# Kernel tuning notes

Hardware: AMD Instinct MI355X
Metric: run time of the kernel (lower is better)

Reference implementation:

```python
import jax, jax.numpy as jnp
import numpy as np
import math

N_HEADS = 16

def _layernorm(x, g, b):
    m = x.mean(-1, keepdims=True)
    v = ((x - m) ** 2).mean(-1, keepdims=True)
    return (x - m) * jax.lax.rsqrt(v + 1e-5) * g + b

def _project(x):
    # Poincare ball (c=1) projection: clip last-dim norm to 1 - eps
    max_norm = 1.0 - 1e-5
    n = jnp.linalg.norm(x, axis=-1, keepdims=True)
    return jnp.where(n > max_norm, x * (max_norm / jnp.maximum(n, 1e-12)), x)


def setup_inputs() -> dict:
    key = jax.random.key(0)
    ks = jax.random.split(key, 8)
    B, L, D = 2, 2048, 1024
    w = lambda k, s: jax.random.normal(k, s, jnp.float32) * 0.02
    return dict(
        x=jax.random.normal(ks[0], (B, L, D), jnp.float32),
        wq=w(ks[1], (D, D)), bq=jnp.zeros((D,), jnp.float32),
        wk=w(ks[2], (D, D)), bk=jnp.zeros((D,), jnp.float32),
        wv=w(ks[3], (D, D)), bv=jnp.zeros((D,), jnp.float32),
        wo=w(ks[4], (D, D)), bo=jnp.zeros((D,), jnp.float32),
        g1=jnp.ones((D,), jnp.float32), b1=jnp.zeros((D,), jnp.float32),
        g2=jnp.ones((D,), jnp.float32), b2=jnp.zeros((D,), jnp.float32),
        w1=w(ks[5], (4 * D, D)), bf1=jnp.zeros((4 * D,), jnp.float32),
        w2=w(ks[6], (D, 4 * D)), bf2=jnp.zeros((D,), jnp.float32),
    )


def reference(x, wq, bq, wk, bk, wv, bv, wo, bo, g1, b1, g2, b2, w1, bf1, w2, bf2):
    B, L, D = x.shape
    H = N_HEADS
    hd = D // H
    temp = math.sqrt(hd)

    xn = _layernorm(x, g1, b1)

    def heads(w, b):
        y = xn @ w.T + b                       # [B, L, D]
        return y.reshape(B, L, H, hd).transpose(0, 2, 1, 3)  # [B, H, L, hd]

    q = _project(heads(wq, bq))
    k = _project(heads(wk, bk))
    v = heads(wv, bv)

    # -||q - k||^2 / temp, via ||q||^2 + ||k||^2 - 2 q.k (same math as the
    # explicit broadcast-diff in the torch code, expressed as a GEMM)
    q2 = (q ** 2).sum(-1)[..., :, None]        # [B, H, L, 1]
    k2 = (k ** 2).sum(-1)[..., None, :]        # [B, H, 1, L]
    qk = jnp.einsum('bhld,bhmd->bhlm', q, k)   # [B, H, L, L]
    scores = -(q2 + k2 - 2.0 * qk) / temp
    attn = jax.nn.softmax(scores, axis=-1)     # dropout = identity (eval mode)

    out = jnp.einsum('bhlm,bhmd->bhld', attn, v)
    out = out.transpose(0, 2, 1, 3).reshape(B, L, D) @ wo.T + bo

    x = _project(x + out)
    xn2 = _layernorm(x, g2, b2)
    h = jax.nn.gelu(xn2 @ w1.T + bf1, approximate=False)  # torch nn.GELU = erf
    x = _project(x + (h @ w2.T + bf2))
    return x
```

## Files before the change

### kernel.cpp

```cpp
#include <hip/hip_runtime.h>
#include <math.h>

#define SEQ_L 2048
#define DM    1024
#define NH    16
#define HD    64
#define BL    4096
#define DFF   4096
#define QKV_S 3072

typedef __attribute__((ext_vector_type(8))) short short8;
typedef __attribute__((ext_vector_type(4))) short s16x4;
typedef __attribute__((ext_vector_type(4))) float f32x4;

__device__ __forceinline__ short f2bf(float x) {
    unsigned u = __float_as_uint(x);
    u += 0x7fff + ((u >> 16) & 1);
    return (short)(u >> 16);
}
__device__ __forceinline__ float bf2f(short s) {
    return __uint_as_float(((unsigned)(unsigned short)s) << 16);
}

__device__ __forceinline__ float gelu_fast(float x) {
    const float xa = fabsf(x);
    const float z = xa * 0.70710678118654752440f;
    const float t = __builtin_amdgcn_rcpf(fmaf(0.3275911f, z, 1.f));
    float P = fmaf(t, 1.061405429f, -1.453152027f);
    P = fmaf(t, P, 1.421413741f);
    P = fmaf(t, P, -0.284496736f);
    P = fmaf(t, P, 0.254829592f);
    P *= t;
    const float e = __expf(-z * z);
    const float erfp = fmaf(-P, e, 1.f);
    return 0.5f * fmaf(xa, erfp, x);
}

__device__ __forceinline__ float block_sum(float v, float* red, int tid) {
#pragma unroll
    for (int m = 32; m; m >>= 1) v += __shfl_xor(v, m);
    if ((tid & 63) == 0) red[tid >> 6] = v;
    __syncthreads();
    v = red[0] + red[1] + red[2] + red[3];
    __syncthreads();
    return v;
}

__global__ __launch_bounds__(256) void cvt6_kernel(
    const float* __restrict__ wq, const float* __restrict__ wk,
    const float* __restrict__ wv, const float* __restrict__ wo,
    const float* __restrict__ w1, const float* __restrict__ w2,
    short* __restrict__ dst) {
    const size_t i = (size_t)blockIdx.x * 256 + threadIdx.x;
    const float* src;
    size_t off;
    if (i < 1048576) {
        const int seg = (int)(i >> 18);
        off = i & 262143;
        src = seg == 0 ? wq : seg == 1 ? wk : seg == 2 ? wv : wo;
    } else if (i < 2097152) { src = w1; off = i - 1048576; }
    else                    { src = w2; off = i - 2097152; }
    const float4 v = ((const float4*)src)[off];
    const s16x4 o = {f2bf(v.x), f2bf(v.y), f2bf(v.z), f2bf(v.w)};
    ((s16x4*)dst)[i] = o;
}

__global__ __launch_bounds__(256) void ln_bf16_kernel(const float* __restrict__ x,
                                                      const float* __restrict__ g,
                                                      const float* __restrict__ b,
                                                      short* __restrict__ out) {
    const int row = blockIdx.x;
    const int tid = threadIdx.x;
    __shared__ float red[4];
    const float4 xv = *(const float4*)(x + (size_t)row * DM + tid * 4);
    float s = xv.x + xv.y + xv.z + xv.w;
    s = block_sum(s, red, tid);
    const float mean = s * (1.f / (float)DM);
    float dx0 = xv.x - mean, dx1 = xv.y - mean, dx2 = xv.z - mean, dx3 = xv.w - mean;
    float ss = dx0 * dx0 + dx1 * dx1 + dx2 * dx2 + dx3 * dx3;
    ss = block_sum(ss, red, tid);
    const float rs = 1.f / sqrtf(ss * (1.f / (float)DM) + 1e-5f);
    const float4 gv = *(const float4*)(g + tid * 4);
    const float4 bv = *(const float4*)(b + tid * 4);
    const s16x4 ob = {f2bf(dx0 * rs * gv.x + bv.x), f2bf(dx1 * rs * gv.y + bv.y),
                      f2bf(dx2 * rs * gv.z + bv.z), f2bf(dx3 * rs * gv.w + bv.w)};
    *(s16x4*)(out + (size_t)row * DM + tid * 4) = ob;
}

__global__ __launch_bounds__(256) void resproj3_kernel(const float* __restrict__ a,
                                                       const float* __restrict__ c0,
                                                       const float* __restrict__ c1,
                                                       float* __restrict__ out) {
    const int row = blockIdx.x;
    const int tid = threadIdx.x;
    __shared__ float red[4];
    const float4 av = *(const float4*)(a + (size_t)row * DM + tid * 4);
    const float4 c0v = *(const float4*)(c0 + (size_t)row * DM + tid * 4);
    const float4 c1v = *(const float4*)(c1 + (size_t)row * DM + tid * 4);
    float4 sv;
    sv.x = av.x + c0v.x + c1v.x;
    sv.y = av.y + c0v.y + c1v.y;
    sv.z = av.z + c0v.z + c1v.z;
    sv.w = av.w + c0v.w + c1v.w;
    float ss = sv.x * sv.x + sv.y * sv.y + sv.z * sv.z + sv.w * sv.w;
    ss = block_sum(ss, red, tid);
    const float n = sqrtf(ss);
    const float mx = 1.f - 1e-5f;
    const float scale = (n > mx) ? (mx / fmaxf(n, 1e-12f)) : 1.f;
    sv.x *= scale; sv.y *= scale; sv.z *= scale; sv.w *= scale;
    *(float4*)(out + (size_t)row * DM + tid * 4) = sv;
}

__global__ __launch_bounds__(256) void qk_prep(const short* __restrict__ qkvB,
                                               short* __restrict__ Qb,
                                               short* __restrict__ Kb,
                                               float* __restrict__ k2) {
    const int tid = threadIdx.x, lane = tid & 63;
    const int vec = blockIdx.x * 4 + (tid >> 6);
    const int row = vec >> 4, h = vec & 15;
    const int b = row >> 11, l = row & 2047;
    const size_t dstv = ((size_t)(b * NH + h) * SEQ_L + l) * HD + lane;
    const float mx = 1.f - 1e-5f;
    {
        const float v = bf2f(qkvB[(size_t)row * QKV_S + h * HD + lane]);
        float s = v * v;
#pragma unroll
        for (int m = 32; m; m >>= 1) s += __shfl_xor(s, m);
        const float n = sqrtf(s);
        const float sc = (n > mx) ? (mx / fmaxf(n, 1e-12f)) : 1.f;
        Qb[dstv] = f2bf(v * sc);
    }
    {
        const float v = bf2f(qkvB[(size_t)row * QKV_S + DM + h * HD + lane]);
        float s = v * v;
#pragma unroll
        for (int m = 32; m; m >>= 1) s += __shfl_xor(s, m);
        const float n = sqrtf(s);
        const float sc = (n > mx) ? (mx / fmaxf(n, 1e-12f)) : 1.f;
        Kb[dstv] = f2bf(v * sc);
        if (lane == 0) k2[(size_t)(b * NH + h) * SEQ_L + l] = s * sc * sc * 0.125f;
    }
}

__global__ __launch_bounds__(256) void v_prep(const short* __restrict__ qkvB,
                                              short* __restrict__ Vtb) {
    const int blk = blockIdx.x;
    const int bh = blk >> 5, kt = blk & 31;
    const int b = bh >> 4, h = bh & 15;
    __shared__ short T[64 * 72];
    const int tid = threadIdx.x;
    {
        const int key = tid >> 2, ch = (tid & 3) * 16;
        const size_t src = ((size_t)b * SEQ_L + kt * 64 + key) * QKV_S + 2 * DM + h * HD + ch;
        *(short8*)&T[key * 72 + ch]     = *(const short8*)(qkvB + src);
        *(short8*)&T[key * 72 + ch + 8] = *(const short8*)(qkvB + src + 8);
    }
    __syncthreads();
    const int hd = tid >> 2, kc = (tid & 3) * 16;
    short8 o0, o1;
#pragma unroll
    for (int j = 0; j < 8; ++j) {
        o0[j] = T[(kc + j) * 72 + hd];
        o1[j] = T[(kc + 8 + j) * 72 + hd];
    }
    short* dst = Vtb + ((size_t)bh * HD + hd) * SEQ_L + kt * 64 + kc;
    *(short8*)dst = o0;
    *(short8*)(dst + 8) = o1;
}

template <int BM, int ACT, int OUTBF, int FUSED, int SWZ>
__global__ __launch_bounds__(256) void gemm_mfma(
    const short* __restrict__ A, const short* __restrict__ Bw,
    const float* __restrict__ bb0, const float* __restrict__ bb1,
    const float* __restrict__ bb2, void* __restrict__ Cout,
    void* __restrict__ Cout1, int M, int N, int K, int Kst) {
    constexpr int RT = BM / 32;
    constexpr bool VEPI = (OUTBF != 0);
    constexpr int SMEM_STAGE = (BM * 32 + 128 * 32) * 2;
    constexpr int SMEM_EPI = 4 * 32 * 72 * 2;
    constexpr int SMEM_BYTES = VEPI ? (SMEM_EPI > SMEM_STAGE ? SMEM_EPI : SMEM_STAGE)
                                    : SMEM_STAGE;
    __shared__ __align__(16) char raw[SMEM_BYTES];
    short* As = (short*)raw;
    short* Bs = As + BM * 32;
    const int tid = threadIdx.x;
    const int wv = tid >> 6, lane = tid & 63;

    int m0, n0;
    if constexpr (SWZ) {
        const int lid = blockIdx.x + gridDim.x * blockIdx.y;
        const int xcd = lid & 7, seq = lid >> 3;
        const int NX = gridDim.x;
        const int mg = gridDim.y >> 3;
        m0 = (xcd * mg + seq / NX) * BM;
        n0 = (seq % NX) * 128;
    } else {
        m0 = blockIdx.y * BM;
        n0 = blockIdx.x * 128;
    }

    const int zz = blockIdx.z;
    const int koff = zz * K;
    const int wr = (wv & 1) * (BM / 2);
    const int wc = (wv >> 1) * 64;

    const int arow = wv * (BM / 4) + (lane >> 2);
    const int brow = wv * 32 + (lane >> 2);
    const short* Ag = A + (size_t)(m0 + arow) * Kst + koff + (lane & 3) * 8;
    const short* Bg = Bw + (size_t)(n0 + brow) * Kst + koff + (lane & 3) * 8;
    short* AsW = As + (wv * (BM / 4)) * 32 + lane * 8;
    short* AsW2 = AsW + 16 * 32;
    short* BsW = Bs + (wv * 32) * 32 + lane * 8;
    short* BsW2 = BsW + 16 * 32;

    const f32x4 z4 = {0.f, 0.f, 0.f, 0.f};
    f32x4 acc[RT][4];
#pragma unroll
    for (int r = 0; r < RT; ++r)
#pragma unroll
        for (int c = 0; c < 4; ++c) acc[r][c] = z4;

    const int lrow = lane & 15, kq = (lane >> 4) * 8;

    short8 ra0, ra1, rb0, rb1;
    ra0 = *(const short8*)(Ag);
    if constexpr (BM == 128) ra1 = *(const short8*)(Ag + (size_t)16 * Kst);
    rb0 = *(const short8*)(Bg);
    rb1 = *(const short8*)(Bg + (size_t)16 * Kst);

    for (int kt = 0; kt < K; kt += 32) {
        __syncthreads();
        *(short8*)AsW = ra0;
        if constexpr (BM == 128) *(short8*)AsW2 = ra1;
        *(short8*)BsW = rb0;
        *(short8*)BsW2 = rb1;
        short8 na0, na1, nb0, nb1;
        if (kt + 32 < K) {
            na0 = *(const short8*)(Ag + kt + 32);
            if constexpr (BM == 128) na1 = *(const short8*)(Ag + (size_t)16 * Kst + kt + 32);
            nb0 = *(const short8*)(Bg + kt + 32);
            nb1 = *(const short8*)(Bg + (size_t)16 * Kst + kt + 32);
        }
        __syncthreads();
        short8 af[RT], bf[4];
#pragma unroll
        for (int r = 0; r < RT; ++r)
            af[r] = *(const short8*)&As[(wr + r * 16 + lrow) * 32 + kq];
#pragma unroll
        for (int c = 0; c < 4; ++c)
            bf[c] = *(const short8*)&Bs[(wc + c * 16 + lrow) * 32 + kq];
#pragma unroll
        for (int r = 0; r < RT; ++r)
#pragma unroll
            for (int c = 0; c < 4; ++c)
                acc[r][c] = __builtin_amdgcn_mfma_f32_16x16x32_bf16(af[r], bf[c], acc[r][c], 0, 0, 0);
        ra0 = na0; ra1 = na1; rb0 = nb0; rb1 = nb1;
    }

    const int col = lane & 15, rb = (lane >> 4) * 4;
    if constexpr (VEPI) {
        __syncthreads();
        short* Ot = (short*)raw + wv * (32 * 72);
        float bias[4];
#pragma unroll
        for (int c = 0; c < 4; ++c) {
            const int gn = n0 + wc + c * 16 + col;
            if constexpr (FUSED) {
                const int seg = gn >> 10;
                bias[c] = (seg == 0 ? bb0 : seg == 1 ? bb1 : bb2)[gn & 1023];
            } else {
                bias[c] = bb0[gn];
            }
        }
        const int erow = lane >> 1, ec = (lane & 1) * 32;
#pragma unroll
        for (int p = 0; p < RT / 2; ++p) {
#pragma unroll
            for (int rr = 0; rr < 2; ++rr) {
                const int r = p * 2 + rr;
#pragma unroll
                for (int c = 0; c < 4; ++c)
#pragma unroll
                    for (int i = 0; i < 4; ++i) {
                        float v = acc[r][c][i] + bias[c];
                        if constexpr (ACT) v = gelu_fast(v);
                        Ot[(rr * 16 + rb + i) * 72 + c * 16 + col] = f2bf(v);
                    }
            }
            const short8 r0 = *(const short8*)&Ot[erow * 72 + ec + 0];
            const short8 r1 = *(const short8*)&Ot[erow * 72 + ec + 8];
            const short8 r2 = *(const short8*)&Ot[erow * 72 + ec + 16];
            const short8 r3 = *(const short8*)&Ot[erow * 72 + ec + 24];
            short* dst = (short*)Cout + (size_t)(m0 + wr + p * 32 + erow) * N + n0 + wc + ec;
            *(short8*)(dst + 0)  = r0;
            *(short8*)(dst + 8)  = r1;
            *(short8*)(dst + 16) = r2;
            *(short8*)(dst + 24) = r3;
        }
    } else {
        float* outp = (float*)(zz ? Cout1 : Cout);
#pragma unroll
        for (int c = 0; c < 4; ++c) {
            const int gn = n0 + wc + c * 16 + col;
            float bias;
            if constexpr (FUSED) {
                const int seg = gn >> 10;
                bias = (seg == 0 ? bb0 : seg == 1 ? bb1 : bb2)[gn & 1023];
            } else {
                bias = bb0[gn];
            }
            if (zz) bias = 0.f;
#pragma unroll
            for (int r = 0; r < RT; ++r) {
                const int gm = m0 + wr + r * 16 + rb;
#pragma unroll
                for (int i = 0; i < 4; ++i) {
                    float v = acc[r][c][i] + bias;
                    if constexpr (ACT) v = gelu_fast(v);
                    outp[(size_t)(gm + i) * N + gn] = v;
                }
            }
        }
    }
}

__global__ __launch_bounds__(256) void attn_mfma2(const short* __restrict__ Qb,
                                                  const short* __restrict__ Kb,
                                                  const short* __restrict__ Vtb,
                                                  const float* __restrict__ k2v,
                                                  short* __restrict__ aO) {
    const int qt = blockIdx.x, h = blockIdx.y, b = blockIdx.z;
    const int tid = threadIdx.x, wv = tid >> 6, lane = tid & 63;
    const int bh = b * NH + h;
    __shared__ __align__(16) short smem[2 * 64 * 72];
    short* Ks = smem;
    short* Vt = smem + 64 * 72;
    const int lrow = lane & 15, q8 = (lane >> 4) * 8, q4 = (lane >> 4) * 4;

    const short* Qh = Qb + (size_t)bh * SEQ_L * HD;
    const short* Kh = Kb + (size_t)bh * SEQ_L * HD;
    const short* Vh = Vtb + (size_t)bh * HD * SEQ_L;
    const float* k2p = k2v + (size_t)bh * SEQ_L;

    short8 qf[2][2];
#pragma unroll
    for (int nt = 0; nt < 2; ++nt)
#pragma unroll
        for (int kc = 0; kc < 2; ++kc)
            qf[nt][kc] = *(const short8*)(Qh +
                (size_t)(qt * 128 + wv * 32 + nt * 16 + lrow) * HD + kc * 32 + q8);

    const f32x4 z4 = {0.f, 0.f, 0.f, 0.f};
    f32x4 o[4][2];
#pragma unroll
    for (int ht = 0; ht < 4; ++ht)
#pragma unroll
        for (int nt = 0; nt < 2; ++nt) o[ht][nt] = z4;
    float lsum[2] = {0.f, 0.f};

    const int srow = tid >> 2, sch = (tid & 3) * 16;

    for (int kt = 0; kt < SEQ_L / 64; ++kt) {
        const int k0 = kt * 64;
        __syncthreads();
        {
            const short* g = Kh + (size_t)(k0 + srow) * HD + sch;
            *(short8*)&Ks[srow * 72 + sch]     = *(const short8*)g;
            *(short8*)&Ks[srow * 72 + sch + 8] = *(const short8*)(g + 8);
            const short* gv = Vh + (size_t)srow * SEQ_L + k0 + sch;
            *(short8*)&Vt[srow * 72 + sch]     = *(const short8*)gv;
            *(short8*)&Vt[srow * 72 + sch + 8] = *(const short8*)(gv + 8);
        }
        __syncthreads();

        short8 p8[2][2];
#pragma unroll
        for (int mt = 0; mt < 4; ++mt) {
            const short8 kf0 = *(const short8*)&Ks[(mt * 16 + lrow) * 72 + q8];
            const short8 kf1 = *(const short8*)&Ks[(mt * 16 + lrow) * 72 + 32 + q8];
            const float4 kk = *(const float4*)(k2p + k0 + mt * 16 + q4);
            const int c = mt >> 1, hi = (mt & 1) * 4;
#pragma unroll
            for (int nt = 0; nt < 2; ++nt) {
                f32x4 s = z4;
                s = __builtin_amdgcn_mfma_f32_16x16x32_bf16(kf0, qf[nt][0], s, 0, 0, 0);
                s = __builtin_amdgcn_mfma_f32_16x16x32_bf16(kf1, qf[nt][1], s, 0, 0, 0);
#pragma unroll
                for (int i = 0; i < 4; ++i) {
                    const float kki = (i == 0) ? kk.x : (i == 1) ? kk.y : (i == 2) ? kk.z : kk.w;
                    const float p = __expf(fmaf(s[i], 0.25f, -kki));
                    lsum[nt] += p;
                    p8[nt][c][hi + i] = f2bf(p);
                }
            }
        }
#pragma unroll
        for (int ht = 0; ht < 4; ++ht) {
#pragma unroll
            for (int c = 0; c < 2; ++c) {
                const s16x4 va = *(const s16x4*)&Vt[(ht * 16 + lrow) * 72 + c * 32 + q4];
                const s16x4 vb = *(const s16x4*)&Vt[(ht * 16 + lrow) * 72 + c * 32 + 16 + q4];
                const short8 v8 = {va[0], va[1], va[2], va[3], vb[0], vb[1], vb[2], vb[3]};
#pragma unroll
                for (int nt = 0; nt < 2; ++nt)
                    o[ht][nt] = __builtin_amdgcn_mfma_f32_16x16x32_bf16(v8, p8[nt][c], o[ht][nt], 0, 0, 0);
            }
        }
    }

#pragma unroll
    for (int nt = 0; nt < 2; ++nt) {
        lsum[nt] += __shfl_xor(lsum[nt], 16);
        lsum[nt] += __shfl_xor(lsum[nt], 32);
    }
    const float inv0 = 1.f / lsum[0], inv1 = 1.f / lsum[1];

    __syncthreads();
    short* Ot = smem + wv * (32 * 72);
#pragma unroll
    for (int ht = 0; ht < 4; ++ht)
#pragma unroll
        for (int nt = 0; nt < 2; ++nt) {
            const float iv = nt ? inv1 : inv0;
            const s16x4 ov = {f2bf(o[ht][nt][0] * iv), f2bf(o[ht][nt][1] * iv),
                              f2bf(o[ht][nt][2] * iv), f2bf(o[ht][nt][3] * iv)};
            *(s16x4*)&Ot[(nt * 16 + lrow) * 72 + ht * 16 + q4] = ov;
        }
    const int erow = lane >> 1, ec = (lane & 1) * 32;
    const short8 r0 = *(const short8*)&Ot[erow * 72 + ec + 0];
    const short8 r1 = *(const short8*)&Ot[erow * 72 + ec + 8];
    const short8 r2 = *(const short8*)&Ot[erow * 72 + ec + 16];
    const short8 r3 = *(const short8*)&Ot[erow * 72 + ec + 24];
    short* dst = aO + ((size_t)b * SEQ_L + qt * 128 + wv * 32 + erow) * DM + h * HD + ec;
    *(short8*)(dst + 0)  = r0;
    *(short8*)(dst + 8)  = r1;
    *(short8*)(dst + 16) = r2;
    *(short8*)(dst + 24) = r3;
}

extern "C" void kernel_launch(void* const* d_in, const int* in_sizes, int n_in,
                              void* d_out, int out_size, void* d_ws, size_t ws_size,
                              hipStream_t stream) {
    const float* x   = (const float*)d_in[0];
    const float* wq  = (const float*)d_in[1];
    const float* bq  = (const float*)d_in[2];
    const float* wk  = (const float*)d_in[3];
    const float* bk  = (const float*)d_in[4];
    const float* wv  = (const float*)d_in[5];
    const float* bv  = (const float*)d_in[6];
    const float* wo  = (const float*)d_in[7];
    const float* bo  = (const float*)d_in[8];
    const float* g1  = (const float*)d_in[9];
    const float* b1  = (const float*)d_in[10];
    const float* g2  = (const float*)d_in[11];
    const float* b2  = (const float*)d_in[12];
    const float* w1  = (const float*)d_in[13];
    const float* bf1 = (const float*)d_in[14];
    const float* w2  = (const float*)d_in[15];
    const float* bf2 = (const float*)d_in[16];
    float* out = (float*)d_out;

    char* base = (char*)d_ws;
    short* wbf  = (short*)base;
    short* qkvB = (short*)(base + (24u << 20));
    short* xnb  = (short*)(base + (48u << 20));
    short* Qb   = xnb;
    short* Kb   = (short*)(base + (56u << 20));
    short* Vtb  = (short*)(base + (64u << 20));
    float* k2   = (float*)(base + (72u << 20));
    short* aO   = (short*)(base + (72u << 20) + (256u << 10));
    float* Pa   = (float*)(base + (24u << 20));
    float* Pb   = (float*)(base + (41u << 20));
    short* xn2b = Vtb;
    short* hbuf = qkvB;
    float* Ya   = (float*)base;
    float* Yb   = (float*)(base + (58u << 20));

    cvt6_kernel<<<12288, 256, 0, stream>>>(wq, wk, wv, wo, w1, w2, wbf);
    ln_bf16_kernel<<<BL, 256, 0, stream>>>(x, g1, b1, xnb);
    gemm_mfma<128, 0, 1, 1, 0><<<dim3(24, 32), 256, 0, stream>>>(
        xnb, wbf, bq, bk, bv, qkvB, nullptr, BL, QKV_S, DM, DM);
    qk_prep<<<16384, 256, 0, stream>>>(qkvB, Qb, Kb, k2);
    v_prep<<<1024, 256, 0, stream>>>(qkvB, Vtb);
    attn_mfma2<<<dim3(16, 16, 2), 256, 0, stream>>>(Qb, Kb, Vtb, k2, aO);
    gemm_mfma<64, 0, 0, 0, 1><<<dim3(8, 64, 2), 256, 0, stream>>>(
        aO, wbf + 3145728, bo, bo, bo, Pa, Pb, BL, DM, DM / 2, DM);
    resproj3_kernel<<<BL, 256, 0, stream>>>(x, Pa, Pb, out);
    ln_bf16_kernel<<<BL, 256, 0, stream>>>(out, g2, b2, xn2b);
    gemm_mfma<128, 1, 1, 0, 0><<<dim3(32, 32), 256, 0, stream>>>(
        xn2b, wbf + 4194304, bf1, bf1, bf1, hbuf, nullptr, BL, DFF, DM, DM);
    gemm_mfma<64, 0, 0, 0, 1><<<dim3(8, 64, 2), 256, 0, stream>>>(
        hbuf, wbf + 8388608, bf2, bf2, bf2, Ya, Yb, BL, DM, DFF / 2, DFF);
    resproj3_kernel<<<BL, 256, 0, stream>>>(out, Ya, Yb, out);
}
```

Baseline: 418.3 us.

## Halve attention query tile, use exp2, MFMA row sums, pre-permute V layout

The attention kernel now handles 64 queries per block, 16 per wave, and launches twice as many blocks. This trades K/V tile reuse for more blocks in flight and fewer registers per wave. Softmax uses exp2 with the scale and log2(e) folded into the constants, and the row sums are computed with an MFMA against a ones vector instead of scalar adds and shuffles. V is written in a permuted layout during prep so the attention kernel reads one short8 from LDS instead of two s16x4 loads.

```diff
diff --git a/kernel.cpp b/kernel.cpp
--- a/kernel.cpp
+++ b/kernel.cpp
@@ -138,7 +138,8 @@
         const float n = sqrtf(s);
         const float sc = (n > mx) ? (mx / fmaxf(n, 1e-12f)) : 1.f;
         Kb[dstv] = f2bf(v * sc);
-        if (lane == 0) k2[(size_t)(b * NH + h) * SEQ_L + l] = s * sc * sc * 0.125f;
+        if (lane == 0)
+            k2[(size_t)(b * NH + h) * SEQ_L + l] = s * sc * sc * 0.18033688011112042f;
     }
 }
 
@@ -163,9 +164,16 @@
         o0[j] = T[(kc + j) * 72 + hd];
         o1[j] = T[(kc + 8 + j) * 72 + hd];
     }
-    short* dst = Vtb + ((size_t)bh * HD + hd) * SEQ_L + kt * 64 + kc;
-    *(short8*)dst = o0;
-    *(short8*)(dst + 8) = o1;
+    const int c = kc >> 5, half = (kc & 16) ? 4 : 0;
+    short* base = Vtb + ((size_t)bh * HD + hd) * SEQ_L + kt * 64 + c * 32 + half;
+    const s16x4 w0 = {o0[0], o0[1], o0[2], o0[3]};
+    const s16x4 w1 = {o0[4], o0[5], o0[6], o0[7]};
+    const s16x4 w2 = {o1[0], o1[1], o1[2], o1[3]};
+    const s16x4 w3 = {o1[4], o1[5], o1[6], o1[7]};
+    *(s16x4*)(base + 0)  = w0;
+    *(s16x4*)(base + 8)  = w1;
+    *(s16x4*)(base + 16) = w2;
+    *(s16x4*)(base + 24) = w3;
 }
 
 template <int BM, int ACT, int OUTBF, int FUSED, int SWZ>
@@ -324,7 +332,7 @@
     }
 }
 
-__global__ __launch_bounds__(256) void attn_mfma2(const short* __restrict__ Qb,
+__global__ __launch_bounds__(256) void attn_mfma3(const short* __restrict__ Qb,
                                                   const short* __restrict__ Kb,
                                                   const short* __restrict__ Vtb,
                                                   const float* __restrict__ k2v,
@@ -342,23 +350,24 @@
     const short* Vh = Vtb + (size_t)bh * HD * SEQ_L;
     const float* k2p = k2v + (size_t)bh * SEQ_L;
 
-    short8 qf[2][2];
-#pragma unroll
-    for (int nt = 0; nt < 2; ++nt)
-#pragma unroll
-        for (int kc = 0; kc < 2; ++kc)
-            qf[nt][kc] = *(const short8*)(Qh +
-                (size_t)(qt * 128 + wv * 32 + nt * 16 + lrow) * HD + kc * 32 + q8);
+    short8 qf[2];
+#pragma unroll
+    for (int kc = 0; kc < 2; ++kc)
+        qf[kc] = *(const short8*)(Qh +
+            (size_t)(qt * 64 + wv * 16 + lrow) * HD + kc * 32 + q8);
+
+    const short one_bf = (short)0x3F80;
+    const short8 ones8 = {one_bf, one_bf, one_bf, one_bf,
+                          one_bf, one_bf, one_bf, one_bf};
 
     const f32x4 z4 = {0.f, 0.f, 0.f, 0.f};
-    f32x4 o[4][2];
-#pragma unroll
-    for (int ht = 0; ht < 4; ++ht)
-#pragma unroll
-        for (int nt = 0; nt < 2; ++nt) o[ht][nt] = z4;
-    float lsum[2] = {0.f, 0.f};
+    f32x4 o[4];
+#pragma unroll
+    for (int ht = 0; ht < 4; ++ht) o[ht] = z4;
+    f32x4 lacc = z4;
 
     const int srow = tid >> 2, sch = (tid & 3) * 16;
+    const float C1 = 0.36067376022224085f;
 
     for (int kt = 0; kt < SEQ_L / 64; ++kt) {
         const int k0 = kt * 64;
@@ -373,69 +382,51 @@
         }
         __syncthreads();
 
-        short8 p8[2][2];
+        short8 p8[2];
 #pragma unroll
         for (int mt = 0; mt < 4; ++mt) {
             const short8 kf0 = *(const short8*)&Ks[(mt * 16 + lrow) * 72 + q8];
             const short8 kf1 = *(const short8*)&Ks[(mt * 16 + lrow) * 72 + 32 + q8];
             const float4 kk = *(const float4*)(k2p + k0 + mt * 16 + q4);
             const int c = mt >> 1, hi = (mt & 1) * 4;
-#pragma unroll
-            for (int nt = 0; nt < 2; ++nt) {
-                f32x4 s = z4;
-                s = __builtin_amdgcn_mfma_f32_16x16x32_bf16(kf0, qf[nt][0], s, 0, 0, 0);
-                s = __builtin_amdgcn_mfma_f32_16x16x32_bf16(kf1, qf[nt][1], s, 0, 0, 0);
-#pragma unroll
-                for (int i = 0; i < 4; ++i) {
-                    const float kki = (i == 0) ? kk.x : (i == 1) ? kk.y : (i == 2) ? kk.z : kk.w;
-                    const float p = __expf(fmaf(s[i], 0.25f, -kki));
-                    lsum[nt] += p;
-                    p8[nt][c][hi + i] = f2bf(p);
-                }
-            }
-        }
+            f32x4 s = z4;
+            s = __builtin_amdgcn_mfma_f32_16x16x32_bf16(kf0, qf[0], s, 0, 0, 0);
+            s = __builtin_amdgcn_mfma_f32_16x16x32_bf16(kf1, qf[1], s, 0, 0, 0);
+#pragma unroll
+            for (int i = 0; i < 4; ++i) {
+                const float kki = (i == 0) ? kk.x : (i == 1) ? kk.y : (i == 2) ? kk.z : kk.w;
+                const float p = __builtin_amdgcn_exp2f(fmaf(s[i], C1, -kki));
+                p8[c][hi + i] = f2bf(p);
+            }
+        }
+        lacc = __builtin_amdgcn_mfma_f32_16x16x32_bf16(ones8, p8[0], lacc, 0, 0, 0);
+        lacc = __builtin_amdgcn_mfma_f32_16x16x32_bf16(ones8, p8[1], lacc, 0, 0, 0);
 #pragma unroll
         for (int ht = 0; ht < 4; ++ht) {
 #pragma unroll
             for (int c = 0; c < 2; ++c) {
-                const s16x4 va = *(const s16x4*)&Vt[(ht * 16 + lrow) * 72 + c * 32 + q4];
-                const s16x4 vb = *(const s16x4*)&Vt[(ht * 16 + lrow) * 72 + c * 32 + 16 + q4];
-                const short8 v8 = {va[0], va[1], va[2], va[3], vb[0], vb[1], vb[2], vb[3]};
-#pragma unroll
-                for (int nt = 0; nt < 2; ++nt)
-                    o[ht][nt] = __builtin_amdgcn_mfma_f32_16x16x32_bf16(v8, p8[nt][c], o[ht][nt], 0, 0, 0);
-            }
-        }
-    }
-
-#pragma unroll
-    for (int nt = 0; nt < 2; ++nt) {
-        lsum[nt] += __shfl_xor(lsum[nt], 16);
-        lsum[nt] += __shfl_xor(lsum[nt], 32);
-    }
-    const float inv0 = 1.f / lsum[0], inv1 = 1.f / lsum[1];
+                const short8 va = *(const short8*)&Vt[(ht * 16 + lrow) * 72 + c * 32 + q8];
+                o[ht] = __builtin_amdgcn_mfma_f32_16x16x32_bf16(va, p8[c], o[ht], 0, 0, 0);
+            }
+        }
+    }
+
+    const float inv = 1.f / lacc[0];
 
     __syncthreads();
-    short* Ot = smem + wv * (32 * 72);
-#pragma unroll
-    for (int ht = 0; ht < 4; ++ht)
-#pragma unroll
-        for (int nt = 0; nt < 2; ++nt) {
-            const float iv = nt ? inv1 : inv0;
-            const s16x4 ov = {f2bf(o[ht][nt][0] * iv), f2bf(o[ht][nt][1] * iv),
-                              f2bf(o[ht][nt][2] * iv), f2bf(o[ht][nt][3] * iv)};
-            *(s16x4*)&Ot[(nt * 16 + lrow) * 72 + ht * 16 + q4] = ov;
-        }
-    const int erow = lane >> 1, ec = (lane & 1) * 32;
+    short* Ot = smem + wv * (16 * 72);
+#pragma unroll
+    for (int ht = 0; ht < 4; ++ht) {
+        const s16x4 ov = {f2bf(o[ht][0] * inv), f2bf(o[ht][1] * inv),
+                          f2bf(o[ht][2] * inv), f2bf(o[ht][3] * inv)};
+        *(s16x4*)&Ot[lrow * 72 + ht * 16 + q4] = ov;
+    }
+    const int erow = lane >> 2, ec = (lane & 3) * 16;
     const short8 r0 = *(const short8*)&Ot[erow * 72 + ec + 0];
     const short8 r1 = *(const short8*)&Ot[erow * 72 + ec + 8];
-    const short8 r2 = *(const short8*)&Ot[erow * 72 + ec + 16];
-    const short8 r3 = *(const short8*)&Ot[erow * 72 + ec + 24];
-    short* dst = aO + ((size_t)b * SEQ_L + qt * 128 + wv * 32 + erow) * DM + h * HD + ec;
-    *(short8*)(dst + 0)  = r0;
-    *(short8*)(dst + 8)  = r1;
-    *(short8*)(dst + 16) = r2;
-    *(short8*)(dst + 24) = r3;
+    short* dst = aO + ((size_t)b * SEQ_L + qt * 64 + wv * 16 + erow) * DM + h * HD + ec;
+    *(short8*)(dst + 0) = r0;
+    *(short8*)(dst + 8) = r1;
 }
 
 extern "C" void kernel_launch(void* const* d_in, const int* in_sizes, int n_in,
@@ -482,7 +473,7 @@
         xnb, wbf, bq, bk, bv, qkvB, nullptr, BL, QKV_S, DM, DM);
     qk_prep<<<16384, 256, 0, stream>>>(qkvB, Qb, Kb, k2);
     v_prep<<<1024, 256, 0, stream>>>(qkvB, Vtb);
-    attn_mfma2<<<dim3(16, 16, 2), 256, 0, stream>>>(Qb, Kb, Vtb, k2, aO);
+    attn_mfma3<<<dim3(32, 16, 2), 256, 0, stream>>>(Qb, Kb, Vtb, k2, aO);
     gemm_mfma<64, 0, 0, 0, 1><<<dim3(8, 64, 2), 256, 0, stream>>>(
         aO, wbf + 3145728, bo, bo, bo, Pa, Pb, BL, DM, DM / 2, DM);
     resproj3_kernel<<<BL, 256, 0, stream>>>(x, Pa, Pb, out);
```

Result: no change. 412.0 us (-1.5%).
